# Kernel optimization log

Measured on AMD Instinct MI355X. Metric: run time of the kernel, lower is better.

Reference implementation:

```python
import jax, jax.numpy as jnp
import numpy as np

N = 50000      # nodes
E = 1_000_000  # edges (avg degree 20)
D = 64         # hidden dim
L = 3          # num dynamics layers
LN_EPS = 1e-5


def layernorm(h, g, b):
    mu = jnp.mean(h, axis=-1, keepdims=True)
    var = jnp.mean(jnp.square(h - mu), axis=-1, keepdims=True)
    return (h - mu) * jax.lax.rsqrt(var + LN_EPS) * g + b


def transformer_conv(h, src, dst, Wq, bq, Wk, bk, Wv, bv, Ws, bs):
    # PyG TransformerConv, heads=1, concat=False, beta=False, root_weight=True
    n = h.shape[0]
    d = Wq.shape[1]
    q = h @ Wq + bq            # [N, D] queries (dst side)
    k = h @ Wk + bk            # [N, D] keys   (src side)
    v = h @ Wv + bv            # [N, D] values (src side)
    logits = jnp.sum(q[dst] * k[src], axis=-1) / jnp.sqrt(jnp.asarray(d, h.dtype))  # [E]
    # segment softmax over incoming edges of each dst node
    m = jax.ops.segment_max(logits, dst, num_segments=n)      # [N]
    e = jnp.exp(logits - m[dst])                               # [E]
    s = jax.ops.segment_sum(e, dst, num_segments=n)            # [N]
    a = e / s[dst]                                             # [E]
    agg = jax.ops.segment_sum(a[:, None] * v[src], dst, num_segments=n)  # [N, D]
    return agg + h @ Ws + bs   # root/skip connection


def setup_inputs() -> dict:
    key = jax.random.key(0)
    ks = jax.random.split(key, 24)
    w = lambda k, shape: (jax.random.normal(k, shape, jnp.float32) * 0.05)
    inp = {
        "x": jax.random.normal(ks[0], (N, D), jnp.float32),
        "edge_index": jax.random.randint(ks[1], (2, E), 0, N, jnp.int32),
        # input_proj conv params
        "Wq0": w(ks[2], (D, D)), "bq0": w(ks[3], (D,)),
        "Wk0": w(ks[4], (D, D)), "bk0": w(ks[5], (D,)),
        "Wv0": w(ks[6], (D, D)), "bv0": w(ks[7], (D,)),
        "Ws0": w(ks[8], (D, D)), "bs0": w(ks[9], (D,)),
        "ln0_g": jnp.ones((D,), jnp.float32), "ln0_b": jnp.zeros((D,), jnp.float32),
        # stacked dynamics conv params [L, ...]
        "Wq": w(ks[10], (L, D, D)), "bq": w(ks[11], (L, D)),
        "Wk": w(ks[12], (L, D, D)), "bk": w(ks[13], (L, D)),
        "Wv": w(ks[14], (L, D, D)), "bv": w(ks[15], (L, D)),
        "Ws": w(ks[16], (L, D, D)), "bs": w(ks[17], (L, D)),
        "ln_g": jnp.ones((L, D), jnp.float32), "ln_b": jnp.zeros((L, D), jnp.float32),
    }
    return inp


def reference(x, edge_index, Wq0, bq0, Wk0, bk0, Wv0, bv0, Ws0, bs0, ln0_g, ln0_b,
              Wq, bq, Wk, bk, Wv, bv, Ws, bs, ln_g, ln_b):
    src, dst = edge_index[0], edge_index[1]
    h = transformer_conv(x, src, dst, Wq0, bq0, Wk0, bk0, Wv0, bv0, Ws0, bs0)
    h = jax.nn.relu(layernorm(h, ln0_g, ln0_b))
    # dropout is identity in eval mode
    for i in range(L):
        hi = transformer_conv(h, src, dst, Wq[i], bq[i], Wk[i], bk[i],
                              Wv[i], bv[i], Ws[i], bs[i])
        h = jax.nn.relu(layernorm(hi + h, ln_g[i], ln_b[i]))
    return h
```

## Files before the change

### kernel.cpp

```cpp
#include <hip/hip_runtime.h>
#include <hip/hip_bf16.h>
#include <math.h>


#define DD 64

typedef __attribute__((ext_vector_type(8))) short short8;
typedef __attribute__((ext_vector_type(4))) float f32x4;

__device__ __forceinline__ float bf_lo(unsigned u) { return __uint_as_float(u << 16); }
__device__ __forceinline__ float bf_hi(unsigned u) { return __uint_as_float(u & 0xffff0000u); }
__device__ __forceinline__ unsigned short f2bf(float f) {
    unsigned u = __float_as_uint(f);
    unsigned r = ((u >> 16) & 1u) + 0x7fffu;
    return (unsigned short)((u + r) >> 16);
}

__global__ void count_rank(const int* __restrict__ dst, int* __restrict__ counts,
                           int* __restrict__ rank, int E) {
    int e = blockIdx.x * blockDim.x + threadIdx.x;
    if (e < E) rank[e] = atomicAdd(&counts[dst[e]], 1);
}

__global__ __launch_bounds__(1024) void scan_local(const int* __restrict__ counts,
                                                   int* __restrict__ localscan,
                                                   int* __restrict__ blockSums, int n) {
    __shared__ int sh[1024];
    int i = blockIdx.x * 1024 + threadIdx.x;
    int val = (i < n) ? counts[i] : 0;
    sh[threadIdx.x] = val;
    __syncthreads();
    for (int off = 1; off < 1024; off <<= 1) {
        int t = (threadIdx.x >= off) ? sh[threadIdx.x - off] : 0;
        __syncthreads();
        sh[threadIdx.x] += t;
        __syncthreads();
    }
    if (i < n) localscan[i] = sh[threadIdx.x] - val;
    if (threadIdx.x == 1023) blockSums[blockIdx.x] = sh[1023];
}

__global__ __launch_bounds__(64) void scan_tops(int* __restrict__ blockSums, int nb) {
    int i = threadIdx.x;
    int val = (i < nb) ? blockSums[i] : 0;
    int s = val;
#pragma unroll
    for (int off = 1; off < 64; off <<= 1) {
        int t = __shfl_up(s, off, 64);
        if (i >= off) s += t;
    }
    if (i < nb) blockSums[i] = s - val;
}

__global__ void emit_rowptr(const int* __restrict__ localscan,
                            const int* __restrict__ blockSums,
                            int* __restrict__ row_ptr, int n, int E) {
    int i = blockIdx.x * blockDim.x + threadIdx.x;
    if (i < n) row_ptr[i] = localscan[i] + blockSums[i >> 10];
    if (i == 0) row_ptr[n] = E;
}

__global__ void scatter_edges(const int* __restrict__ src, const int* __restrict__ dst,
                              const int* __restrict__ rank, const int* __restrict__ row_ptr,
                              int* __restrict__ col, int E) {
    int e = blockIdx.x * blockDim.x + threadIdx.x;
    if (e < E) col[row_ptr[dst[e]] + rank[e]] = src[e];
}

__global__ void prep_all(const float* __restrict__ x, unsigned short* __restrict__ hbf,
                         int nD,
                         const float* __restrict__ W0, const float* __restrict__ W1,
                         const float* __restrict__ W2, const float* __restrict__ W3,
                         const float* __restrict__ Wqs, const float* __restrict__ Wks,
                         const float* __restrict__ Wvs, const float* __restrict__ Wss,
                         unsigned short* __restrict__ Wt) {
    int i = blockIdx.x * blockDim.x + threadIdx.x;
    if (i < nD) { hbf[i] = f2bf(x[i]); return; }
    int id = i - nD;
    if (id >= 16 * 4096) return;
    int mat = id >> 12, rem = id & 4095;
    int nn = rem >> 6, kk = rem & 63;
    int layer = mat >> 2, wh = mat & 3;
    const float* W;
    if (layer == 0) W = wh == 0 ? W0 : wh == 1 ? W1 : wh == 2 ? W2 : W3;
    else {
        const float* base = wh == 0 ? Wqs : wh == 1 ? Wks : wh == 2 ? Wvs : Wss;
        W = base + (size_t)(layer - 1) * 4096;
    }
    Wt[id] = f2bf(W[kk * 64 + nn]);
}

__global__ __launch_bounds__(256) void gemm_mfma(
    const unsigned short* __restrict__ hbf, const unsigned short* __restrict__ Wt,
    const float* __restrict__ Bq, const float* __restrict__ Bk,
    const float* __restrict__ Bv, const float* __restrict__ Bs,
    float* __restrict__ qO, unsigned short* __restrict__ kO,
    unsigned short* __restrict__ vO, float* __restrict__ sO, int ntiles) {
    int lane = threadIdx.x & 63;
    int wave = threadIdx.x >> 6;
    int ml = lane & 15, ql = lane >> 4;

    const unsigned short* W = Wt + wave * 4096;
    short8 wfrag[4][2];
#pragma unroll
    for (int t = 0; t < 4; ++t)
#pragma unroll
        for (int kh = 0; kh < 2; ++kh)
            wfrag[t][kh] = *(const short8*)(W + (t * 16 + ml) * 64 + kh * 32 + ql * 8);

    const float* bias = wave == 0 ? Bq : wave == 1 ? Bk : wave == 2 ? Bv : Bs;
    float4 bias4[4];
#pragma unroll
    for (int t = 0; t < 4; ++t) bias4[t] = *(const float4*)(bias + t * 16 + ql * 4);

    for (int tile = blockIdx.x; tile < ntiles; tile += gridDim.x) {
        int node0 = tile * 16;
        short8 hfrag[2];
#pragma unroll
        for (int kh = 0; kh < 2; ++kh)
            hfrag[kh] = *(const short8*)(hbf + (size_t)(node0 + ml) * 64 + kh * 32 + ql * 8);
        f32x4 acc[4];
#pragma unroll
        for (int t = 0; t < 4; ++t) {
            acc[t][0] = bias4[t].x; acc[t][1] = bias4[t].y;
            acc[t][2] = bias4[t].z; acc[t][3] = bias4[t].w;
        }
#pragma unroll
        for (int t = 0; t < 4; ++t)
#pragma unroll
            for (int kh = 0; kh < 2; ++kh)
                acc[t] = __builtin_amdgcn_mfma_f32_16x16x32_bf16(
                    wfrag[t][kh], hfrag[kh], acc[t], 0, 0, 0);

        size_t rowoff = (size_t)(node0 + ml) * 64;
        if (wave == 0 || wave == 3) {
            float* O = (wave == 0) ? qO : sO;
#pragma unroll
            for (int t = 0; t < 4; ++t) {
                float4 st = {acc[t][0], acc[t][1], acc[t][2], acc[t][3]};
                *(float4*)(O + rowoff + t * 16 + ql * 4) = st;
            }
        } else {
            unsigned short* O = (wave == 1) ? kO : vO;
#pragma unroll
            for (int t = 0; t < 4; ++t) {
                uint2 st;
                st.x = (unsigned)f2bf(acc[t][0]) | ((unsigned)f2bf(acc[t][1]) << 16);
                st.y = (unsigned)f2bf(acc[t][2]) | ((unsigned)f2bf(acc[t][3]) << 16);
                *(uint2*)(O + rowoff + t * 16 + ql * 4) = st;
            }
        }
    }
}

__global__ __launch_bounds__(256) void attn_agg_ln(
    const float* __restrict__ q, const unsigned short* __restrict__ k,
    const unsigned short* __restrict__ v, const float* __restrict__ sk,
    const float* __restrict__ hprev,
    const int* __restrict__ row_ptr, const int* __restrict__ col,
    const float* __restrict__ g, const float* __restrict__ b,
    float* __restrict__ out, unsigned short* __restrict__ hbf_out, int n) {
    int node = blockIdx.x * 4 + (threadIdx.x >> 6);
    int lane = threadIdx.x & 63;
    if (node >= n) return;
    int grp = lane >> 3;
    int qi = lane & 7;

    size_t rowb = (size_t)node * DD + qi * 8;
    float4 qa = *(const float4*)(q + rowb);
    float4 qb4 = *(const float4*)(q + rowb + 4);
    qa.x *= 0.125f; qa.y *= 0.125f; qa.z *= 0.125f; qa.w *= 0.125f;
    qb4.x *= 0.125f; qb4.y *= 0.125f; qb4.z *= 0.125f; qb4.w *= 0.125f;
    int beg = row_ptr[node], end = row_ptr[node + 1];

    float ssum = 0.0f;
    float4 aa = {0.f, 0.f, 0.f, 0.f}, ab = {0.f, 0.f, 0.f, 0.f};

    for (int e0 = beg; e0 < end; e0 += 8) {
        int e = e0 + grp;
        if (e < end) {
            int s = col[e];
            size_t sb = (size_t)s * DD + qi * 8;
            uint4 ku = *(const uint4*)(k + sb);
            uint4 vu = *(const uint4*)(v + sb);
            float d = qa.x * bf_lo(ku.x) + qa.y * bf_hi(ku.x)
                    + qa.z * bf_lo(ku.y) + qa.w * bf_hi(ku.y)
                    + qb4.x * bf_lo(ku.z) + qb4.y * bf_hi(ku.z)
                    + qb4.z * bf_lo(ku.w) + qb4.w * bf_hi(ku.w);
            d += __shfl_xor(d, 1);
            d += __shfl_xor(d, 2);
            d += __shfl_xor(d, 4);
            float p = __expf(d);
            ssum += p;
            aa.x += p * bf_lo(vu.x); aa.y += p * bf_hi(vu.x);
            aa.z += p * bf_lo(vu.y); aa.w += p * bf_hi(vu.y);
            ab.x += p * bf_lo(vu.z); ab.y += p * bf_hi(vu.z);
            ab.z += p * bf_lo(vu.w); ab.w += p * bf_hi(vu.w);
        }
    }

#pragma unroll
    for (int off = 8; off <= 32; off <<= 1) {
        ssum += __shfl_xor(ssum, off);
        aa.x += __shfl_xor(aa.x, off); aa.y += __shfl_xor(aa.y, off);
        aa.z += __shfl_xor(aa.z, off); aa.w += __shfl_xor(aa.w, off);
        ab.x += __shfl_xor(ab.x, off); ab.y += __shfl_xor(ab.y, off);
        ab.z += __shfl_xor(ab.z, off); ab.w += __shfl_xor(ab.w, off);
    }
    float inv = (end > beg) ? 1.0f / ssum : 0.0f;
    aa.x *= inv; aa.y *= inv; aa.z *= inv; aa.w *= inv;
    ab.x *= inv; ab.y *= inv; ab.z *= inv; ab.w *= inv;

    float4 s4a = *(const float4*)(sk + rowb);
    float4 s4b = *(const float4*)(sk + rowb + 4);
    aa.x += s4a.x; aa.y += s4a.y; aa.z += s4a.z; aa.w += s4a.w;
    ab.x += s4b.x; ab.y += s4b.y; ab.z += s4b.z; ab.w += s4b.w;
    if (hprev) {
        float4 h4a = *(const float4*)(hprev + rowb);
        float4 h4b = *(const float4*)(hprev + rowb + 4);
        aa.x += h4a.x; aa.y += h4a.y; aa.z += h4a.z; aa.w += h4a.w;
        ab.x += h4b.x; ab.y += h4b.y; ab.z += h4b.z; ab.w += h4b.w;
    }

    float s1 = aa.x + aa.y + aa.z + aa.w + ab.x + ab.y + ab.z + ab.w;
    s1 += __shfl_xor(s1, 1);
    s1 += __shfl_xor(s1, 2);
    s1 += __shfl_xor(s1, 4);
    float mu = s1 * (1.0f / DD);
    float dx0 = aa.x - mu, dx1 = aa.y - mu, dx2 = aa.z - mu, dx3 = aa.w - mu;
    float dx4 = ab.x - mu, dx5 = ab.y - mu, dx6 = ab.z - mu, dx7 = ab.w - mu;
    float s2v = dx0 * dx0 + dx1 * dx1 + dx2 * dx2 + dx3 * dx3
              + dx4 * dx4 + dx5 * dx5 + dx6 * dx6 + dx7 * dx7;
    s2v += __shfl_xor(s2v, 1);
    s2v += __shfl_xor(s2v, 2);
    s2v += __shfl_xor(s2v, 4);
    float var = s2v * (1.0f / DD);
    float is = rsqrtf(var + 1e-5f);
    float4 g4a = *(const float4*)(g + qi * 8);
    float4 g4b = *(const float4*)(g + qi * 8 + 4);
    float4 b4a = *(const float4*)(b + qi * 8);
    float4 b4b = *(const float4*)(b + qi * 8 + 4);
    float4 ya, yb;
    ya.x = fmaxf(dx0 * is * g4a.x + b4a.x, 0.0f);
    ya.y = fmaxf(dx1 * is * g4a.y + b4a.y, 0.0f);
    ya.z = fmaxf(dx2 * is * g4a.z + b4a.z, 0.0f);
    ya.w = fmaxf(dx3 * is * g4a.w + b4a.w, 0.0f);
    yb.x = fmaxf(dx4 * is * g4b.x + b4b.x, 0.0f);
    yb.y = fmaxf(dx5 * is * g4b.y + b4b.y, 0.0f);
    yb.z = fmaxf(dx6 * is * g4b.z + b4b.z, 0.0f);
    yb.w = fmaxf(dx7 * is * g4b.w + b4b.w, 0.0f);
    if (grp == 0) {
        *(float4*)(out + rowb) = ya;
        *(float4*)(out + rowb + 4) = yb;
        uint4 hv;
        hv.x = (unsigned)f2bf(ya.x) | ((unsigned)f2bf(ya.y) << 16);
        hv.y = (unsigned)f2bf(ya.z) | ((unsigned)f2bf(ya.w) << 16);
        hv.z = (unsigned)f2bf(yb.x) | ((unsigned)f2bf(yb.y) << 16);
        hv.w = (unsigned)f2bf(yb.z) | ((unsigned)f2bf(yb.w) << 16);
        *(uint4*)(hbf_out + rowb) = hv;
    }
}

extern "C" void kernel_launch(void* const* d_in, const int* in_sizes, int n_in,
                              void* d_out, int out_size, void* d_ws, size_t ws_size,
                              hipStream_t stream) {
    const int D = DD;
    const float* x = (const float*)d_in[0];
    const int n = in_sizes[0] / D;
    const int* ei = (const int*)d_in[1];
    const int E = in_sizes[1] / 2;
    const int* srcp = ei;
    const int* dstp = ei + E;

    char* wsp = (char*)d_ws;
    auto take = [&](size_t bytes) {
        char* p = wsp;
        wsp += (bytes + 255) & ~(size_t)255;
        return (void*)p;
    };
    int* counts    = (int*)take((size_t)n * 4);
    int* row_ptr   = (int*)take((size_t)(n + 1) * 4);
    int* rank      = (int*)take((size_t)E * 4);
    int* col       = (int*)take((size_t)E * 4);
    int* localscan = (int*)take((size_t)n * 4);
    int* blockSums = (int*)take((size_t)1024 * 4);
    size_t fsz = (size_t)n * D * 4;
    float* qb          = (float*)take(fsz);
    unsigned short* kb = (unsigned short*)take(fsz / 2);
    unsigned short* vb = (unsigned short*)take(fsz / 2);
    float* sb          = (float*)take(fsz);
    float* hA          = (float*)take(fsz);
    float* hB          = (float*)take(fsz);
    unsigned short* hbf = (unsigned short*)take(fsz / 2);
    unsigned short* Wt  = (unsigned short*)take((size_t)16 * 4096 * 2);

    hipMemsetAsync(counts, 0, (size_t)n * 4, stream);
    int tb = 256;
    int nbScan = (n + 1023) / 1024;
    count_rank<<<(E + tb - 1) / tb, tb, 0, stream>>>(dstp, counts, rank, E);
    scan_local<<<nbScan, 1024, 0, stream>>>(counts, localscan, blockSums, n);
    scan_tops<<<1, 64, 0, stream>>>(blockSums, nbScan);
    emit_rowptr<<<(n + tb - 1) / tb, tb, 0, stream>>>(localscan, blockSums, row_ptr, n, E);
    scatter_edges<<<(E + tb - 1) / tb, tb, 0, stream>>>(srcp, dstp, rank, row_ptr, col, E);

    int prep_total = n * D + 16 * 4096;
    prep_all<<<(prep_total + 255) / 256, 256, 0, stream>>>(
        x, hbf, n * D,
        (const float*)d_in[2], (const float*)d_in[4], (const float*)d_in[6],
        (const float*)d_in[8], (const float*)d_in[12], (const float*)d_in[14],
        (const float*)d_in[16], (const float*)d_in[18], Wt);

    const float* h = x;
    int ntiles = n / 16;
    int nba = (n + 3) / 4;
    for (int layer = 0; layer < 4; ++layer) {
        const float *bq_, *bk_, *bv_, *bs_, *g_, *b_;
        if (layer == 0) {
            bq_ = (const float*)d_in[3];  bk_ = (const float*)d_in[5];
            bv_ = (const float*)d_in[7];  bs_ = (const float*)d_in[9];
            g_  = (const float*)d_in[10]; b_  = (const float*)d_in[11];
        } else {
            int i = layer - 1;
            bq_ = (const float*)d_in[13] + (size_t)i * D;
            bk_ = (const float*)d_in[15] + (size_t)i * D;
            bv_ = (const float*)d_in[17] + (size_t)i * D;
            bs_ = (const float*)d_in[19] + (size_t)i * D;
            g_  = (const float*)d_in[20] + (size_t)i * D;
            b_  = (const float*)d_in[21] + (size_t)i * D;
        }
        gemm_mfma<<<512, 256, 0, stream>>>(hbf, Wt + (size_t)layer * 4 * 4096,
                                           bq_, bk_, bv_, bs_,
                                           qb, kb, vb, sb, ntiles);
        float* hout = (layer == 3) ? (float*)d_out : ((layer & 1) ? hB : hA);
        attn_agg_ln<<<nba, 256, 0, stream>>>(qb, kb, vb, sb,
                                             layer == 0 ? nullptr : h,
                                             row_ptr, col, g_, b_, hout, hbf, n);
        h = hout;
    }
}
```

Measured before the change: 419.1 us.

## Switch to fp16 with interleaved K/V rows, prefetched column indices and fused residual

Changes activations and weights from bf16 to fp16 and uses fp16 MFMA and packed fdot2 for the attention logits. K and V are interleaved into a single 128-wide row, addressed by a pre-shifted byte offset stored in col, so one gather reaches both. Q is stored in fp16 with the 1/sqrt(d) scale folded into the weights and bias, and the residual add moves into the GEMM's skip-output wave. The next column index is prefetched in the aggregation loop. Together these reduce gather bytes and per-edge ALU work, at the cost of fp16 range and precision risk, and src<<8 overflows if N grows past about 8M.

New measurement: 393.9 us. 1.06x faster.

```diff
diff --git a/kernel.cpp b/kernel.cpp
--- a/kernel.cpp
+++ b/kernel.cpp
@@ -1,19 +1,32 @@
 #include <hip/hip_runtime.h>
-#include <hip/hip_bf16.h>
 #include <math.h>
 
 
 #define DD 64
 
-typedef __attribute__((ext_vector_type(8))) short short8;
+typedef __attribute__((ext_vector_type(8))) _Float16 h8;
+typedef __attribute__((ext_vector_type(2))) _Float16 h2;
 typedef __attribute__((ext_vector_type(4))) float f32x4;
 
-__device__ __forceinline__ float bf_lo(unsigned u) { return __uint_as_float(u << 16); }
-__device__ __forceinline__ float bf_hi(unsigned u) { return __uint_as_float(u & 0xffff0000u); }
-__device__ __forceinline__ unsigned short f2bf(float f) {
-    unsigned u = __float_as_uint(f);
-    unsigned r = ((u >> 16) & 1u) + 0x7fffu;
-    return (unsigned short)((u + r) >> 16);
+__device__ __forceinline__ unsigned short f2h(float f) {
+    union { _Float16 h; unsigned short u; } c;
+    c.h = (_Float16)f;
+    return c.u;
+}
+__device__ __forceinline__ h2 u2h2(unsigned u) {
+    union { unsigned u; h2 h; } c; c.u = u; return c.h;
+}
+__device__ __forceinline__ unsigned pk2u(float a, float b) {
+    union { decltype(__builtin_amdgcn_cvt_pkrtz(0.f, 0.f)) h; unsigned u; } c;
+    c.h = __builtin_amdgcn_cvt_pkrtz(a, b);
+    return c.u;
+}
+__device__ __forceinline__ float h2dot(h2 a, h2 b, float c) {
+#if __has_builtin(__builtin_amdgcn_fdot2)
+    return __builtin_amdgcn_fdot2(a, b, c, false);
+#else
+    return fmaf((float)a[0], (float)b[0], fmaf((float)a[1], (float)b[1], c));
+#endif
 }
 
 __global__ void count_rank(const int* __restrict__ dst, int* __restrict__ counts,
@@ -64,7 +77,7 @@
                               const int* __restrict__ rank, const int* __restrict__ row_ptr,
                               int* __restrict__ col, int E) {
     int e = blockIdx.x * blockDim.x + threadIdx.x;
-    if (e < E) col[row_ptr[dst[e]] + rank[e]] = src[e];
+    if (e < E) col[row_ptr[dst[e]] + rank[e]] = src[e] << 8;
 }
 
 __global__ void prep_all(const float* __restrict__ x, unsigned short* __restrict__ hbf,
@@ -75,7 +88,7 @@
                          const float* __restrict__ Wvs, const float* __restrict__ Wss,
                          unsigned short* __restrict__ Wt) {
     int i = blockIdx.x * blockDim.x + threadIdx.x;
-    if (i < nD) { hbf[i] = f2bf(x[i]); return; }
+    if (i < nD) { hbf[i] = f2h(x[i]); return; }
     int id = i - nD;
     if (id >= 16 * 4096) return;
     int mat = id >> 12, rem = id & 4095;
@@ -87,38 +100,47 @@
         const float* base = wh == 0 ? Wqs : wh == 1 ? Wks : wh == 2 ? Wvs : Wss;
         W = base + (size_t)(layer - 1) * 4096;
     }
-    Wt[id] = f2bf(W[kk * 64 + nn]);
+    float val = W[kk * 64 + nn];
+    if (wh == 0) val *= 0.125f;
+    Wt[id] = f2h(val);
 }
 
 __global__ __launch_bounds__(256) void gemm_mfma(
     const unsigned short* __restrict__ hbf, const unsigned short* __restrict__ Wt,
     const float* __restrict__ Bq, const float* __restrict__ Bk,
     const float* __restrict__ Bv, const float* __restrict__ Bs,
-    float* __restrict__ qO, unsigned short* __restrict__ kO,
-    unsigned short* __restrict__ vO, float* __restrict__ sO, int ntiles) {
+    const float* __restrict__ hprev,
+    unsigned short* __restrict__ qO, unsigned short* __restrict__ kvO,
+    float* __restrict__ sO, int ntiles) {
     int lane = threadIdx.x & 63;
     int wave = threadIdx.x >> 6;
     int ml = lane & 15, ql = lane >> 4;
 
     const unsigned short* W = Wt + wave * 4096;
-    short8 wfrag[4][2];
+    h8 wfrag[4][2];
 #pragma unroll
     for (int t = 0; t < 4; ++t)
 #pragma unroll
         for (int kh = 0; kh < 2; ++kh)
-            wfrag[t][kh] = *(const short8*)(W + (t * 16 + ml) * 64 + kh * 32 + ql * 8);
+            wfrag[t][kh] = *(const h8*)(W + (t * 16 + ml) * 64 + kh * 32 + ql * 8);
 
     const float* bias = wave == 0 ? Bq : wave == 1 ? Bk : wave == 2 ? Bv : Bs;
     float4 bias4[4];
 #pragma unroll
-    for (int t = 0; t < 4; ++t) bias4[t] = *(const float4*)(bias + t * 16 + ql * 4);
+    for (int t = 0; t < 4; ++t) {
+        bias4[t] = *(const float4*)(bias + t * 16 + ql * 4);
+        if (wave == 0) {
+            bias4[t].x *= 0.125f; bias4[t].y *= 0.125f;
+            bias4[t].z *= 0.125f; bias4[t].w *= 0.125f;
+        }
+    }
 
     for (int tile = blockIdx.x; tile < ntiles; tile += gridDim.x) {
         int node0 = tile * 16;
-        short8 hfrag[2];
+        h8 hfrag[2];
 #pragma unroll
         for (int kh = 0; kh < 2; ++kh)
-            hfrag[kh] = *(const short8*)(hbf + (size_t)(node0 + ml) * 64 + kh * 32 + ql * 8);
+            hfrag[kh] = *(const h8*)(hbf + (size_t)(node0 + ml) * 64 + kh * 32 + ql * 8);
         f32x4 acc[4];
 #pragma unroll
         for (int t = 0; t < 4; ++t) {
@@ -129,34 +151,44 @@
         for (int t = 0; t < 4; ++t)
 #pragma unroll
             for (int kh = 0; kh < 2; ++kh)
-                acc[t] = __builtin_amdgcn_mfma_f32_16x16x32_bf16(
+                acc[t] = __builtin_amdgcn_mfma_f32_16x16x32_f16(
                     wfrag[t][kh], hfrag[kh], acc[t], 0, 0, 0);
 
-        size_t rowoff = (size_t)(node0 + ml) * 64;
-        if (wave == 0 || wave == 3) {
-            float* O = (wave == 0) ? qO : sO;
+        size_t rowe = (size_t)(node0 + ml) * 64;
+        if (wave == 0) {
+#pragma unroll
+            for (int t = 0; t < 4; ++t) {
+                uint2 st;
+                st.x = pk2u(acc[t][0], acc[t][1]);
+                st.y = pk2u(acc[t][2], acc[t][3]);
+                *(uint2*)(qO + rowe + t * 16 + ql * 4) = st;
+            }
+        } else if (wave == 3) {
 #pragma unroll
             for (int t = 0; t < 4; ++t) {
                 float4 st = {acc[t][0], acc[t][1], acc[t][2], acc[t][3]};
-                *(float4*)(O + rowoff + t * 16 + ql * 4) = st;
+                if (hprev) {
+                    float4 h4 = *(const float4*)(hprev + rowe + t * 16 + ql * 4);
+                    st.x += h4.x; st.y += h4.y; st.z += h4.z; st.w += h4.w;
+                }
+                *(float4*)(sO + rowe + t * 16 + ql * 4) = st;
             }
         } else {
-            unsigned short* O = (wave == 1) ? kO : vO;
+            size_t kve = (size_t)(node0 + ml) * 128 + (wave == 2 ? 64 : 0);
 #pragma unroll
             for (int t = 0; t < 4; ++t) {
                 uint2 st;
-                st.x = (unsigned)f2bf(acc[t][0]) | ((unsigned)f2bf(acc[t][1]) << 16);
-                st.y = (unsigned)f2bf(acc[t][2]) | ((unsigned)f2bf(acc[t][3]) << 16);
-                *(uint2*)(O + rowoff + t * 16 + ql * 4) = st;
+                st.x = pk2u(acc[t][0], acc[t][1]);
+                st.y = pk2u(acc[t][2], acc[t][3]);
+                *(uint2*)(kvO + kve + t * 16 + ql * 4) = st;
             }
         }
     }
 }
 
 __global__ __launch_bounds__(256) void attn_agg_ln(
-    const float* __restrict__ q, const unsigned short* __restrict__ k,
-    const unsigned short* __restrict__ v, const float* __restrict__ sk,
-    const float* __restrict__ hprev,
+    const unsigned short* __restrict__ qh, const unsigned short* __restrict__ kv,
+    const float* __restrict__ sk,
     const int* __restrict__ row_ptr, const int* __restrict__ col,
     const float* __restrict__ g, const float* __restrict__ b,
     float* __restrict__ out, unsigned short* __restrict__ hbf_out, int n) {
@@ -166,36 +198,43 @@
     int grp = lane >> 3;
     int qi = lane & 7;
 
-    size_t rowb = (size_t)node * DD + qi * 8;
-    float4 qa = *(const float4*)(q + rowb);
-    float4 qb4 = *(const float4*)(q + rowb + 4);
-    qa.x *= 0.125f; qa.y *= 0.125f; qa.z *= 0.125f; qa.w *= 0.125f;
-    qb4.x *= 0.125f; qb4.y *= 0.125f; qb4.z *= 0.125f; qb4.w *= 0.125f;
+    size_t ro = (size_t)node * DD + qi * 8;
+    uint4 qu = *(const uint4*)(qh + ro);
+    float4 s4a = *(const float4*)(sk + ro);
+    float4 s4b = *(const float4*)(sk + ro + 4);
     int beg = row_ptr[node], end = row_ptr[node + 1];
 
     float ssum = 0.0f;
     float4 aa = {0.f, 0.f, 0.f, 0.f}, ab = {0.f, 0.f, 0.f, 0.f};
-
+    const char* kvb = (const char*)kv;
+
+    int e = beg + grp;
+    int cv = (e < end) ? col[e] : -1;
     for (int e0 = beg; e0 < end; e0 += 8) {
-        int e = e0 + grp;
-        if (e < end) {
-            int s = col[e];
-            size_t sb = (size_t)s * DD + qi * 8;
-            uint4 ku = *(const uint4*)(k + sb);
-            uint4 vu = *(const uint4*)(v + sb);
-            float d = qa.x * bf_lo(ku.x) + qa.y * bf_hi(ku.x)
-                    + qa.z * bf_lo(ku.y) + qa.w * bf_hi(ku.y)
-                    + qb4.x * bf_lo(ku.z) + qb4.y * bf_hi(ku.z)
-                    + qb4.z * bf_lo(ku.w) + qb4.w * bf_hi(ku.w);
+        bool act = cv >= 0;
+        uint4 ku, vu;
+        if (act) {
+            const uint4* kp = (const uint4*)(kvb + cv) + qi;
+            ku = kp[0];
+            vu = kp[8];
+        }
+        e += 8;
+        cv = (e < end) ? col[e] : -1;
+        if (act) {
+            float d = h2dot(u2h2(qu.x), u2h2(ku.x), 0.0f);
+            d = h2dot(u2h2(qu.y), u2h2(ku.y), d);
+            d = h2dot(u2h2(qu.z), u2h2(ku.z), d);
+            d = h2dot(u2h2(qu.w), u2h2(ku.w), d);
             d += __shfl_xor(d, 1);
             d += __shfl_xor(d, 2);
             d += __shfl_xor(d, 4);
             float p = __expf(d);
             ssum += p;
-            aa.x += p * bf_lo(vu.x); aa.y += p * bf_hi(vu.x);
-            aa.z += p * bf_lo(vu.y); aa.w += p * bf_hi(vu.y);
-            ab.x += p * bf_lo(vu.z); ab.y += p * bf_hi(vu.z);
-            ab.z += p * bf_lo(vu.w); ab.w += p * bf_hi(vu.w);
+            h2 v0 = u2h2(vu.x), v1 = u2h2(vu.y), v2 = u2h2(vu.z), v3 = u2h2(vu.w);
+            aa.x = fmaf((float)v0[0], p, aa.x); aa.y = fmaf((float)v0[1], p, aa.y);
+            aa.z = fmaf((float)v1[0], p, aa.z); aa.w = fmaf((float)v1[1], p, aa.w);
+            ab.x = fmaf((float)v2[0], p, ab.x); ab.y = fmaf((float)v2[1], p, ab.y);
+            ab.z = fmaf((float)v3[0], p, ab.z); ab.w = fmaf((float)v3[1], p, ab.w);
         }
     }
 
@@ -211,16 +250,8 @@
     aa.x *= inv; aa.y *= inv; aa.z *= inv; aa.w *= inv;
     ab.x *= inv; ab.y *= inv; ab.z *= inv; ab.w *= inv;
 
-    float4 s4a = *(const float4*)(sk + rowb);
-    float4 s4b = *(const float4*)(sk + rowb + 4);
     aa.x += s4a.x; aa.y += s4a.y; aa.z += s4a.z; aa.w += s4a.w;
     ab.x += s4b.x; ab.y += s4b.y; ab.z += s4b.z; ab.w += s4b.w;
-    if (hprev) {
-        float4 h4a = *(const float4*)(hprev + rowb);
-        float4 h4b = *(const float4*)(hprev + rowb + 4);
-        aa.x += h4a.x; aa.y += h4a.y; aa.z += h4a.z; aa.w += h4a.w;
-        ab.x += h4b.x; ab.y += h4b.y; ab.z += h4b.z; ab.w += h4b.w;
-    }
 
     float s1 = aa.x + aa.y + aa.z + aa.w + ab.x + ab.y + ab.z + ab.w;
     s1 += __shfl_xor(s1, 1);
@@ -250,14 +281,14 @@
     yb.z = fmaxf(dx6 * is * g4b.z + b4b.z, 0.0f);
     yb.w = fmaxf(dx7 * is * g4b.w + b4b.w, 0.0f);
     if (grp == 0) {
-        *(float4*)(out + rowb) = ya;
-        *(float4*)(out + rowb + 4) = yb;
+        *(float4*)(out + ro) = ya;
+        *(float4*)(out + ro + 4) = yb;
         uint4 hv;
-        hv.x = (unsigned)f2bf(ya.x) | ((unsigned)f2bf(ya.y) << 16);
-        hv.y = (unsigned)f2bf(ya.z) | ((unsigned)f2bf(ya.w) << 16);
-        hv.z = (unsigned)f2bf(yb.x) | ((unsigned)f2bf(yb.y) << 16);
-        hv.w = (unsigned)f2bf(yb.z) | ((unsigned)f2bf(yb.w) << 16);
-        *(uint4*)(hbf_out + rowb) = hv;
+        hv.x = pk2u(ya.x, ya.y);
+        hv.y = pk2u(ya.z, ya.w);
+        hv.z = pk2u(yb.x, yb.y);
+        hv.w = pk2u(yb.z, yb.w);
+        *(uint4*)(hbf_out + ro) = hv;
     }
 }
 
@@ -285,12 +316,11 @@
     int* localscan = (int*)take((size_t)n * 4);
     int* blockSums = (int*)take((size_t)1024 * 4);
     size_t fsz = (size_t)n * D * 4;
-    float* qb          = (float*)take(fsz);
-    unsigned short* kb = (unsigned short*)take(fsz / 2);
-    unsigned short* vb = (unsigned short*)take(fsz / 2);
-    float* sb          = (float*)take(fsz);
-    float* hA          = (float*)take(fsz);
-    float* hB          = (float*)take(fsz);
+    unsigned short* qb  = (unsigned short*)take(fsz / 2);
+    unsigned short* kvb = (unsigned short*)take(fsz);
+    float* sb           = (float*)take(fsz);
+    float* hA           = (float*)take(fsz);
+    float* hB           = (float*)take(fsz);
     unsigned short* hbf = (unsigned short*)take(fsz / 2);
     unsigned short* Wt  = (unsigned short*)take((size_t)16 * 4096 * 2);
 
@@ -330,10 +360,10 @@
         }
         gemm_mfma<<<512, 256, 0, stream>>>(hbf, Wt + (size_t)layer * 4 * 4096,
                                            bq_, bk_, bv_, bs_,
-                                           qb, kb, vb, sb, ntiles);
+                                           layer == 0 ? nullptr : h,
+                                           qb, kvb, sb, ntiles);
         float* hout = (layer == 3) ? (float*)d_out : ((layer & 1) ? hB : hA);
-        attn_agg_ln<<<nba, 256, 0, stream>>>(qb, kb, vb, sb,
-                                             layer == 0 ? nullptr : h,
+        attn_agg_ln<<<nba, 256, 0, stream>>>(qb, kvb, sb,
                                              row_ptr, col, g_, b_, hout, hbf, n);
         h = hout;
     }
```
